# Kernel optimization log

Measured on AMD Instinct MI355X. Metric: run time of the kernel, lower is better.

The kernel has to match this reference:

```python
import jax, jax.numpy as jnp
import numpy as np

D_MODEL = 2048
N_HEADS = 16
D_HEAD = 128
INIT_RANGE = 0.02
EPSILON = -100000.0  # mask fill value from the original module


def setup_inputs() -> dict:
    key = jax.random.key(0)
    ks = jax.random.split(key, 6)
    x = jax.random.normal(ks[0], (2, 2048, D_MODEL), dtype=jnp.float32)
    W_Q = jax.random.normal(ks[1], (N_HEADS, D_MODEL, D_HEAD), dtype=jnp.float32) * INIT_RANGE
    W_K = jax.random.normal(ks[2], (N_HEADS, D_MODEL, D_HEAD), dtype=jnp.float32) * INIT_RANGE
    W_V = jax.random.normal(ks[3], (N_HEADS, D_MODEL, D_HEAD), dtype=jnp.float32) * INIT_RANGE
    W_O = jax.random.normal(ks[4], (N_HEADS, D_HEAD, D_MODEL), dtype=jnp.float32) * INIT_RANGE
    b_Q = jnp.zeros((N_HEADS, D_HEAD), dtype=jnp.float32)
    b_K = jnp.zeros((N_HEADS, D_HEAD), dtype=jnp.float32)
    b_V = jnp.zeros((N_HEADS, D_HEAD), dtype=jnp.float32)
    b_O = jnp.zeros((D_MODEL,), dtype=jnp.float32)
    return {"normalized_resid_pre": x, "W_Q": W_Q, "b_Q": b_Q, "W_K": W_K,
            "b_K": b_K, "W_V": W_V, "b_V": b_V, "W_O": W_O, "b_O": b_O}


def reference(normalized_resid_pre, W_Q, b_Q, W_K, b_K, W_V, b_V, W_O, b_O):
    x = normalized_resid_pre  # [b, s, d_model]
    # per-head projections: [b, s, h, d_head]
    q = jnp.einsum('bsd,hdk->bshk', x, W_Q) + b_Q
    k = jnp.einsum('bsd,hdk->bshk', x, W_K) + b_K
    v = jnp.einsum('bsd,hdk->bshk', x, W_V) + b_V
    # attention scores [b, h, q, k]
    scores = jnp.einsum('bqhk,bshk->bhqs', q, k) / jnp.sqrt(jnp.float32(D_HEAD))
    S = scores.shape[-1]
    causal = jnp.tril(jnp.ones((S, S), dtype=bool))  # True = keep
    scores = jnp.where(causal, scores, jnp.float32(EPSILON))
    pattern = jax.nn.softmax(scores, axis=-1)
    z = jnp.einsum('bhqs,bshk->bqhk', pattern, v)
    attn_out = jnp.einsum('bqhk,hkd->bqd', z, W_O) + b_O
    return attn_out
```

## Files before the change

### kernel.cpp

```cpp
#include <hip/hip_runtime.h>
#include <hip/hip_bf16.h>

typedef unsigned short bfu;
typedef short          bf16x8 __attribute__((ext_vector_type(8)));
typedef float          floatx4 __attribute__((ext_vector_type(4)));
typedef unsigned short bfu4 __attribute__((ext_vector_type(4)));
typedef unsigned int   u32x2 __attribute__((ext_vector_type(2)));

__device__ __forceinline__ bfu f2bf(float f) {
    __hip_bfloat16 h = __float2bfloat16(f);
    return __builtin_bit_cast(unsigned short, h);
}

__device__ __forceinline__ float ex2(float x) {
#if __has_builtin(__builtin_amdgcn_exp2f)
    return __builtin_amdgcn_exp2f(x);
#else
    return exp2f(x);
#endif
}

__device__ __forceinline__ void glds16(const bfu* g, bfu* l) {
    __builtin_amdgcn_global_load_lds(
        (const __attribute__((address_space(1))) unsigned int*)g,
        (__attribute__((address_space(3))) unsigned int*)l, 16, 0, 0);
}

#define BATCH 2
#define SEQ   2048
#define DM    2048
#define NH    16
#define DKH   128
#define SCALE  0.08838834764831845f
#define SCALEQ 0.1275174245f

__global__ __launch_bounds__(256)
void cvt_x(const float* __restrict__ x, bfu* __restrict__ xb, int n) {
    const int i = (blockIdx.x * 256 + threadIdx.x) * 4;
    if (i >= n) return;
    const float4 v = *(const float4*)(x + i);
    bfu4 p; p[0] = f2bf(v.x); p[1] = f2bf(v.y); p[2] = f2bf(v.z); p[3] = f2bf(v.w);
    *(bfu4*)(xb + i) = p;
}

__device__ __forceinline__ void t64(const float* __restrict__ src,
                                    bfu* __restrict__ dst,
                                    int C, int r0, int c0, float s,
                                    float (*tile)[65]) {
    const int t  = threadIdx.x;
    const int lr = t >> 4;
    const int lc = (t & 15) * 4;
    #pragma unroll
    for (int pp = 0; pp < 4; pp++) {
        const float4 v = *(const float4*)(src + (size_t)(r0 + pp*16 + lr) * C + c0 + lc);
        tile[pp*16 + lr][lc + 0] = v.x;
        tile[pp*16 + lr][lc + 1] = v.y;
        tile[pp*16 + lr][lc + 2] = v.z;
        tile[pp*16 + lr][lc + 3] = v.w;
    }
    __syncthreads();
    const int rc = t & 15;
    const int cb = t >> 4;
    #pragma unroll
    for (int pp = 0; pp < 4; pp++) {
        const int c = pp*16 + cb;
        bfu4 pk;
        #pragma unroll
        for (int j = 0; j < 4; j++) pk[j] = f2bf(tile[rc*4 + j][c] * s);
        *(bfu4*)(dst + (size_t)(c0 + c) * DM + r0 + rc*4) = pk;
    }
}

__global__ __launch_bounds__(256)
void tcvt_qkv64(const float* __restrict__ WQ, const float* __restrict__ WK,
                const float* __restrict__ WV,
                bfu* __restrict__ WtQ, bfu* __restrict__ WtK, bfu* __restrict__ WtV) {
    __shared__ float tile[64][65];
    const int z = blockIdx.z;
    const int p = z >> 4, h = z & 15;
    const float* src = ((p == 0) ? WQ : (p == 1) ? WK : WV) + (size_t)h * DM * DKH;
    bfu*         dst = ((p == 0) ? WtQ : (p == 1) ? WtK : WtV) + (size_t)h * DKH * DM;
    const float  s   = (p == 0) ? SCALEQ : 1.0f;
    t64(src, dst, DKH, blockIdx.y * 64, blockIdx.x * 64, s, tile);
}

__global__ __launch_bounds__(256)
void tcvt_wo64(const float* __restrict__ WO, bfu* __restrict__ WtO) {
    __shared__ float tile[64][65];
    t64(WO, WtO, DM, blockIdx.y * 64, blockIdx.x * 64, 1.0f, tile);
}

__device__ __forceinline__ void stg_half(const bfu* gbase, bfu* slot,
                                         int wave, int lane, int csw) {
    #pragma unroll
    for (int l = 0; l < 2; l++) {
        const int j = l * 8 + wave;
        glds16(gbase + (size_t)((j >> 1) * 16 + (lane >> 2)) * DM
                     + (j & 1) * 32 + csw,
               slot + j * 512);
    }
}

__device__ __forceinline__ void ld_b8(bf16x8 (&bv)[4][2], const bfu* slot, int rdo) {
    #pragma unroll
    for (int n = 0; n < 4; n++)
        #pragma unroll
        for (int ks = 0; ks < 2; ks++)
            bv[n][ks] = *(const bf16x8*)&slot[(n * 2 + ks) * 512 + rdo];
}

__device__ __forceinline__ void ld_a8(bf16x8 (&af)[4][2], const bfu* slot, int rdo) {
    #pragma unroll
    for (int m = 0; m < 4; m++)
        #pragma unroll
        for (int ks = 0; ks < 2; ks++)
            af[m][ks] = *(const bf16x8*)&slot[(m * 2 + ks) * 512 + rdo];
}

template<int MH, int NHALF>
__device__ __forceinline__ void mfma16(floatx4 (&acc)[8][4],
                                       const bf16x8 (&af)[4][2],
                                       const bf16x8 (&bv)[4][2]) {
    __builtin_amdgcn_s_setprio(1);
    #pragma unroll
    for (int m = 0; m < 4; m++)
        #pragma unroll
        for (int n = 0; n < 2; n++)
            #pragma unroll
            for (int ks = 0; ks < 2; ks++)
                acc[MH*4 + m][NHALF*2 + n] =
                    __builtin_amdgcn_mfma_f32_16x16x32_bf16(
                        af[m][ks], bv[NHALF*2 + n][ks],
                        acc[MH*4 + m][NHALF*2 + n], 0, 0, 0);
    __builtin_amdgcn_s_setprio(0);
}

#define BARW()                                                      \
    __builtin_amdgcn_s_barrier();                                   \
    asm volatile("s_waitcnt lgkmcnt(0)" ::: "memory");              \
    __builtin_amdgcn_sched_barrier(0)

__global__ __launch_bounds__(512, 2)
void proj_qk8(const bfu* __restrict__ xb,
              const bfu* __restrict__ WtQ, const bfu* __restrict__ WtK,
              const float* __restrict__ bQ, const float* __restrict__ bK,
              bfu* __restrict__ Qall, bfu* __restrict__ Kall) {
    __shared__ __align__(16) bfu As[2][2][8192];
    __shared__ __align__(16) bfu Bs[2][2][8192];

    const int p = blockIdx.y >> 3;
    const bfu*   Wt   = (p == 0) ? WtQ : WtK;
    const float* bias = (p == 0) ? bQ  : bK;
    const float  bscale = (p == 0) ? SCALEQ : 1.0f;

    const int tid  = threadIdx.x;
    const int lane = tid & 63;
    const int wave = tid >> 6;
    const int lrow = lane & 15;
    const int quad = lane >> 4;
    const int wr   = wave >> 2;
    const int wc   = wave & 3;
    const size_t m0 = (size_t)blockIdx.x * 256;
    const int    n0 = (int)(blockIdx.y & 7) * 256;

    const int csw = ((lane & 3) * 8) ^ ((lane & 32) ? 16 : 0);
    const int rdo = lrow * 32 + ((quad * 8) ^ ((lrow & 8) ? 16 : 0));

    const bfu* Ab = xb + m0 * DM;
    const bfu* Bb = Wt + (size_t)n0 * DM;

    floatx4 acc[8][4] = {};
    bf16x8 af[4][2], bv[4][2];

#define STAGE_A(tau, h)                                                     \
    if ((tau) < 32) stg_half(Ab + (size_t)((h) * 128) * DM + (tau) * 64,    \
                             &As[(tau) & 1][h][0], wave, lane, csw)
#define STAGE_B(tau, h)                                                     \
    if ((tau) < 32) stg_half(Bb + (size_t)((h) * 128) * DM + (tau) * 64,    \
                             &Bs[(tau) & 1][h][0], wave, lane, csw)

    STAGE_B(0, 0); STAGE_B(0, 1); STAGE_A(0, 0); STAGE_A(0, 1);
    STAGE_B(1, 0); STAGE_B(1, 1); STAGE_A(1, 0);
    asm volatile("s_waitcnt vmcnt(6)" ::: "memory");
    __builtin_amdgcn_s_barrier();

    #pragma unroll 1
    for (int i = 0; i < 16; i++) {
        const int t0 = 2 * i;
        ld_b8(bv, &Bs[0][wc >> 1][(wc & 1) * 4096], rdo);
        ld_a8(af, &As[0][wr][0], rdo);
        STAGE_A(t0 + 1, 1);
        BARW();
        mfma16<0, 0>(acc, af, bv);
        __builtin_amdgcn_s_barrier();
        STAGE_B(t0 + 2, 0);
        BARW();
        mfma16<0, 1>(acc, af, bv);
        __builtin_amdgcn_s_barrier();
        ld_a8(af, &As[0][wr][4096], rdo);
        STAGE_B(t0 + 2, 1);
        BARW();
        mfma16<1, 0>(acc, af, bv);
        __builtin_amdgcn_s_barrier();
        STAGE_A(t0 + 2, 0);
        BARW();
        mfma16<1, 1>(acc, af, bv);
        if (i == 15) asm volatile("s_waitcnt vmcnt(0)" ::: "memory");
        else         asm volatile("s_waitcnt vmcnt(6)" ::: "memory");
        __builtin_amdgcn_s_barrier();
        ld_b8(bv, &Bs[1][wc >> 1][(wc & 1) * 4096], rdo);
        ld_a8(af, &As[1][wr][0], rdo);
        STAGE_A(t0 + 2, 1);
        BARW();
        mfma16<0, 0>(acc, af, bv);
        __builtin_amdgcn_s_barrier();
        STAGE_B(t0 + 3, 0);
        BARW();
        mfma16<0, 1>(acc, af, bv);
        __builtin_amdgcn_s_barrier();
        ld_a8(af, &As[1][wr][4096], rdo);
        STAGE_B(t0 + 3, 1);
        BARW();
        mfma16<1, 0>(acc, af, bv);
        __builtin_amdgcn_s_barrier();
        STAGE_A(t0 + 3, 0);
        BARW();
        mfma16<1, 1>(acc, af, bv);
        if (i < 15) asm volatile("s_waitcnt vmcnt(6)" ::: "memory");
        __builtin_amdgcn_s_barrier();
    }
#undef STAGE_A
#undef STAGE_B

    bfu* Out = (p == 0) ? Qall : Kall;
    #pragma unroll
    for (int m = 0; m < 8; m++) {
        #pragma unroll
        for (int n = 0; n < 4; n++) {
            const int gn = n0 + wc * 64 + n * 16 + lrow;
            const float bvv = bias[gn] * bscale;
            #pragma unroll
            for (int r = 0; r < 4; r++) {
                const size_t gm = m0 + wr * 128 + m * 16 + quad * 4 + r;
                Out[gm * DM + gn] = f2bf(acc[m][n][r] + bvv);
            }
        }
    }
}

__global__ __launch_bounds__(256)
void proj_v(const bfu* __restrict__ xb, const bfu* __restrict__ WtV,
            const float* __restrict__ bV, bfu* __restrict__ Vt) {
    __shared__ bfu As[128 * 32];
    __shared__ bfu Bs[128 * 32];
    const int tid  = threadIdx.x;
    const int lane = tid & 63;
    const int wave = tid >> 6;
    const int lrow = lane & 15;
    const int quad = lane >> 4;
    const int mw = (wave & 1) * 64;
    const int nw = (wave >> 1) * 64;
    const size_t m0 = (size_t)blockIdx.x * 128;
    const size_t n0 = (size_t)blockIdx.y * 128;
    const int rowb = lane >> 2;
    const int colb = (lane & 3) * 8;

    floatx4 acc[4][4] = {};

    for (int k0 = 0; k0 < DM; k0 += 32) {
        __syncthreads();
        #pragma unroll
        for (int i = 0; i < 2; i++) {
            const int rg = wave * 2 + i;
            glds16(xb  + (m0 + rg*16 + rowb) * DM + k0 + colb, &As[rg * 512]);
            glds16(WtV + (n0 + rg*16 + rowb) * DM + k0 + colb, &Bs[rg * 512]);
        }
        __syncthreads();
        bf16x8 af[4], bfr[4];
        #pragma unroll
        for (int t = 0; t < 4; t++) {
            af[t]  = *(const bf16x8*)&As[(mw + t*16 + lrow) * 32 + quad * 8];
            bfr[t] = *(const bf16x8*)&Bs[(nw + t*16 + lrow) * 32 + quad * 8];
        }
        #pragma unroll
        for (int mt = 0; mt < 4; mt++)
            #pragma unroll
            for (int nt = 0; nt < 4; nt++)
                acc[mt][nt] = __builtin_amdgcn_mfma_f32_16x16x32_bf16(
                                  af[mt], bfr[nt], acc[mt][nt], 0, 0, 0);
    }

    #pragma unroll
    for (int mt = 0; mt < 4; mt++) {
        #pragma unroll
        for (int nt = 0; nt < 4; nt++) {
            const int nl = (int)n0 + nw + nt*16 + lrow;
            const float bvv = bV[nl];
            const size_t gm0 = m0 + mw + mt*16 + quad*4;
            const int b = (int)(gm0 >> 11), s = (int)(gm0 & 2047);
            bfu4 pk;
            #pragma unroll
            for (int r = 0; r < 4; r++) pk[r] = f2bf(acc[mt][nt][r] + bvv);
            *(bfu4*)&Vt[((size_t)(b * NH + (nl >> 7)) * DKH + (nl & 127)) * SEQ + s] = pk;
        }
    }
}

__global__ __launch_bounds__(256)
void flash_attn(const bfu* __restrict__ Q, const bfu* __restrict__ K,
                const bfu* __restrict__ Vt, bfu* __restrict__ Z) {
    __shared__ bfu Ks[4][64][32];
    __shared__ bfu Vs[2][128][32];
    __shared__ bfu Ps[4][16][72];

    const int tid  = threadIdx.x;
    const int lane = tid & 63;
    const int wave = tid >> 6;
    const int lrow = lane & 15;
    const int quad = lane >> 4;
    const int hb = blockIdx.x;
    const int h = hb & 15, b = hb >> 4;
    const int qt = 31 - blockIdx.y;
    const int q0w = qt * 64 + wave * 16;
    const int rowb = lane >> 2;
    const int csw  = ((lane & 3) * 8) ^ ((lane & 32) ? 16 : 0);
    const int rq0  = (quad * 8) ^ ((lrow & 8) ? 16 : 0);

    const bfu* Qrow = Q + (size_t)(b * SEQ + q0w + lrow) * DM + h * DKH;
    bf16x8 qf[4];
    #pragma unroll
    for (int kc = 0; kc < 4; kc++)
        qf[kc] = *(const bf16x8*)(Qrow + kc*32 + quad*8);

    floatx4 z[8] = {};
    float l_loc = 0.f;
    const int qg = q0w + lrow;

    const bfu* Kb = K + (size_t)b * SEQ * DM + h * DKH;
    const bfu* Vb = Vt + (size_t)(b * NH + h) * DKH * SEQ;
    const int ntiles = qt + 1;

    for (int it = 0; it < ntiles; it++) {
        const int s0 = it * 64;
        __syncthreads();
        #pragma unroll
        for (int i = 0; i < 8; i++) {
            const int chunk = wave * 8 + i;
            if (chunk < 16) {
                const int kc = chunk >> 2, kg = chunk & 3;
                glds16(Kb + (size_t)(s0 + kg*16 + rowb) * DM + kc*32 + csw,
                       &Ks[kc][kg*16][0]);
            } else {
                const int c2 = chunk - 16;
                const int sh = c2 >> 3, dg = c2 & 7;
                glds16(Vb + (size_t)(dg*16 + rowb) * SEQ + s0 + sh*32 + csw,
                       &Vs[sh][dg*16][0]);
            }
        }
        __syncthreads();

        floatx4 sc[4];
        __builtin_amdgcn_s_setprio(1);
        #pragma unroll
        for (int st = 0; st < 4; st++) {
            floatx4 a = {};
            #pragma unroll
            for (int kc = 0; kc < 4; kc++) {
                bf16x8 kf = *(const bf16x8*)&Ks[kc][st*16 + lrow][rq0];
                a = __builtin_amdgcn_mfma_f32_16x16x32_bf16(kf, qf[kc], a, 0, 0, 0);
            }
            sc[st] = a;
        }
        __builtin_amdgcn_s_setprio(0);

        if (it + 1 < ntiles) {
            #pragma unroll
            for (int st = 0; st < 4; st++) {
                const float p0 = ex2(sc[st][0]);
                const float p1 = ex2(sc[st][1]);
                const float p2 = ex2(sc[st][2]);
                const float p3 = ex2(sc[st][3]);
                l_loc += (p0 + p1) + (p2 + p3);
                u32x2 pk;
                pk[0] = (unsigned)f2bf(p0) | ((unsigned)f2bf(p1) << 16);
                pk[1] = (unsigned)f2bf(p2) | ((unsigned)f2bf(p3) << 16);
                *(u32x2*)&Ps[wave][lrow][st*16 + quad*4] = pk;
            }
        } else {
            #pragma unroll
            for (int st = 0; st < 4; st++) {
                const int sbase = s0 + st*16 + quad*4;
                const float p0 = (sbase + 0 <= qg) ? ex2(sc[st][0]) : 0.f;
                const float p1 = (sbase + 1 <= qg) ? ex2(sc[st][1]) : 0.f;
                const float p2 = (sbase + 2 <= qg) ? ex2(sc[st][2]) : 0.f;
                const float p3 = (sbase + 3 <= qg) ? ex2(sc[st][3]) : 0.f;
                l_loc += (p0 + p1) + (p2 + p3);
                u32x2 pk;
                pk[0] = (unsigned)f2bf(p0) | ((unsigned)f2bf(p1) << 16);
                pk[1] = (unsigned)f2bf(p2) | ((unsigned)f2bf(p3) << 16);
                *(u32x2*)&Ps[wave][lrow][st*16 + quad*4] = pk;
            }
        }

        bf16x8 pf0 = *(const bf16x8*)&Ps[wave][lrow][quad*8];
        bf16x8 pf1 = *(const bf16x8*)&Ps[wave][lrow][32 + quad*8];
        __builtin_amdgcn_s_setprio(1);
        #pragma unroll
        for (int dt = 0; dt < 8; dt++) {
            bf16x8 v0 = *(const bf16x8*)&Vs[0][dt*16 + lrow][rq0];
            z[dt] = __builtin_amdgcn_mfma_f32_16x16x32_bf16(pf0, v0, z[dt], 0, 0, 0);
            bf16x8 v1 = *(const bf16x8*)&Vs[1][dt*16 + lrow][rq0];
            z[dt] = __builtin_amdgcn_mfma_f32_16x16x32_bf16(pf1, v1, z[dt], 0, 0, 0);
        }
        __builtin_amdgcn_s_setprio(0);
    }

    float L = l_loc;
    L += __shfl_xor(L, 16);
    L += __shfl_xor(L, 32);
    float inv[4];
    #pragma unroll
    for (int r = 0; r < 4; r++)
        inv[r] = 1.0f / __shfl(L, quad*4 + r, 64);
    #pragma unroll
    for (int dt = 0; dt < 8; dt++) {
        #pragma unroll
        for (int r = 0; r < 4; r++) {
            const int qq = q0w + quad*4 + r;
            const int dk = dt*16 + lrow;
            Z[(size_t)(b * SEQ + qq) * DM + h * DKH + dk] = f2bf(z[dt][r] * inv[r]);
        }
    }
}

__global__ __launch_bounds__(256)
void out_gemm(const bfu* __restrict__ Zb, const bfu* __restrict__ WtO,
              const float* __restrict__ bO, float* out) {
    __shared__ bfu As[128 * 32];
    __shared__ bfu Bs[128 * 32];
    const int tid  = threadIdx.x;
    const int lane = tid & 63;
    const int wave = tid >> 6;
    const int lrow = lane & 15;
    const int quad = lane >> 4;
    const int mw = (wave & 1) * 64;
    const int nw = (wave >> 1) * 64;
    const size_t m0 = (size_t)blockIdx.x * 128;
    const size_t n0 = (size_t)blockIdx.y * 128;
    const int rowb = lane >> 2, colb = (lane & 3) * 8;

    floatx4 acc[4][4] = {};

    for (int k0 = 0; k0 < DM; k0 += 32) {
        __syncthreads();
        #pragma unroll
        for (int i = 0; i < 2; i++) {
            const int rg = wave * 2 + i;
            glds16(Zb  + (m0 + rg*16 + rowb) * DM + k0 + colb, &As[rg * 512]);
            glds16(WtO + (n0 + rg*16 + rowb) * DM + k0 + colb, &Bs[rg * 512]);
        }
        __syncthreads();
        bf16x8 af[4], bfr[4];
        #pragma unroll
        for (int t = 0; t < 4; t++) {
            af[t]  = *(const bf16x8*)&As[(mw + t*16 + lrow) * 32 + quad * 8];
            bfr[t] = *(const bf16x8*)&Bs[(nw + t*16 + lrow) * 32 + quad * 8];
        }
        #pragma unroll
        for (int mt = 0; mt < 4; mt++)
            #pragma unroll
            for (int nt = 0; nt < 4; nt++)
                acc[mt][nt] = __builtin_amdgcn_mfma_f32_16x16x32_bf16(
                                  af[mt], bfr[nt], acc[mt][nt], 0, 0, 0);
    }

    #pragma unroll
    for (int mt = 0; mt < 4; mt++) {
        #pragma unroll
        for (int nt = 0; nt < 4; nt++) {
            const size_t gn = n0 + nw + nt*16 + lrow;
            const float bv = bO[gn];
            #pragma unroll
            for (int r = 0; r < 4; r++) {
                const size_t gm = m0 + mw + mt*16 + quad*4 + r;
                out[gm * DM + gn] = acc[mt][nt][r] + bv;
            }
        }
    }
}

extern "C" void kernel_launch(void* const* d_in, const int* in_sizes, int n_in,
                              void* d_out, int out_size, void* d_ws, size_t ws_size,
                              hipStream_t stream) {
    const float* x  = (const float*)d_in[0];
    const float* WQ = (const float*)d_in[1];
    const float* bQ = (const float*)d_in[2];
    const float* WK = (const float*)d_in[3];
    const float* bK = (const float*)d_in[4];
    const float* WV = (const float*)d_in[5];
    const float* bV = (const float*)d_in[6];
    const float* WO = (const float*)d_in[7];
    const float* bO = (const float*)d_in[8];
    float* out = (float*)d_out;
    bfu* ws  = (bfu*)d_ws;
    bfu* dob = (bfu*)d_out;

    bfu* Qall = ws;
    bfu* Kall = Qall + 8388608;
    bfu* Vt   = Kall + 8388608;
    bfu* Zb   = Vt   + 8388608;
    bfu* WtV  = Zb;
    bfu* xb   = dob;
    bfu* WtQ  = dob + 8388608;
    bfu* WtK  = dob + 12582912;

    cvt_x<<<8192, 256, 0, stream>>>(x, xb, BATCH * SEQ * DM);

    tcvt_qkv64<<<dim3(2, 32, 48), 256, 0, stream>>>(WQ, WK, WV, WtQ, WtK, WtV);

    proj_qk8<<<dim3(16, 16), 512, 0, stream>>>(xb, WtQ, WtK, bQ, bK, Qall, Kall);
    proj_v<<<dim3(32, 16), 256, 0, stream>>>(xb, WtV, bV, Vt);

    flash_attn<<<dim3(32, 32), 256, 0, stream>>>(Qall, Kall, Vt, Zb);

    tcvt_wo64<<<dim3(32, 32), 256, 0, stream>>>(WO, Qall);
    out_gemm<<<dim3(32, 16), 256, 0, stream>>>(Zb, Qall, bO, out);
}
```

Measured before the change: 360.6 us.

## Merge input conversion kernels and fuse Q/K/V projections into one launch

Combines the x conversion and the Q/K/V weight transpose-convert into a single `prep` launch, dispatched by block index. It also merges the Q/K projection GEMM and the V projection GEMM into one 512-block `proj_qkv` launch. The V path is retiled to use 512 threads with 128x256 tiles in its own shared buffers. The goal is to cut launch overhead and let the V GEMM run alongside the Q/K GEMM instead of after it. The risk is that the fused kernel's static shared memory grows from 64KB to about 88KB per block, which may stop two blocks from fitting per CU.

```diff
diff --git a/kernel.cpp b/kernel.cpp
--- a/kernel.cpp
+++ b/kernel.cpp
@@ -35,32 +35,39 @@
 #define SCALEQ 0.1275174245f
 
 __global__ __launch_bounds__(256)
-void cvt_x(const float* __restrict__ x, bfu* __restrict__ xb, int n) {
-    const int i = (blockIdx.x * 256 + threadIdx.x) * 4;
-    if (i >= n) return;
-    const float4 v = *(const float4*)(x + i);
-    bfu4 p; p[0] = f2bf(v.x); p[1] = f2bf(v.y); p[2] = f2bf(v.z); p[3] = f2bf(v.w);
-    *(bfu4*)(xb + i) = p;
-}
-
-__device__ __forceinline__ void t64(const float* __restrict__ src,
-                                    bfu* __restrict__ dst,
-                                    int C, int r0, int c0, float s,
-                                    float (*tile)[65]) {
+void prep(const float* __restrict__ x, bfu* __restrict__ xb,
+          const float* __restrict__ WQ, const float* __restrict__ WK,
+          const float* __restrict__ WV,
+          bfu* __restrict__ WtQ, bfu* __restrict__ WtK, bfu* __restrict__ WtV) {
+    __shared__ float tile[64][65];
+    const int bid = blockIdx.x;
+    if (bid < 8192) {
+        const int i = (bid * 256 + threadIdx.x) * 4;
+        const float4 v = *(const float4*)(x + i);
+        bfu4 p; p[0] = f2bf(v.x); p[1] = f2bf(v.y); p[2] = f2bf(v.z); p[3] = f2bf(v.w);
+        *(bfu4*)(xb + i) = p;
+        return;
+    }
+    const int idx = bid - 8192;
+    const int gx = idx & 1, gy = (idx >> 1) & 31, gz = idx >> 6;
+    const int p = gz >> 4, h = gz & 15;
+    const float* src = ((p == 0) ? WQ : (p == 1) ? WK : WV) + (size_t)h * DM * DKH;
+    bfu*         dst = ((p == 0) ? WtQ : (p == 1) ? WtK : WtV) + (size_t)h * DKH * DM;
+    const float  s   = (p == 0) ? SCALEQ : 1.0f;
+    const int r0 = gy * 64, c0 = gx * 64;
     const int t  = threadIdx.x;
     const int lr = t >> 4;
     const int lc = (t & 15) * 4;
     #pragma unroll
     for (int pp = 0; pp < 4; pp++) {
-        const float4 v = *(const float4*)(src + (size_t)(r0 + pp*16 + lr) * C + c0 + lc);
+        const float4 v = *(const float4*)(src + (size_t)(r0 + pp*16 + lr) * DKH + c0 + lc);
         tile[pp*16 + lr][lc + 0] = v.x;
         tile[pp*16 + lr][lc + 1] = v.y;
         tile[pp*16 + lr][lc + 2] = v.z;
         tile[pp*16 + lr][lc + 3] = v.w;
     }
     __syncthreads();
-    const int rc = t & 15;
-    const int cb = t >> 4;
+    const int rc = t & 15, cb = t >> 4;
     #pragma unroll
     for (int pp = 0; pp < 4; pp++) {
         const int c = pp*16 + cb;
@@ -72,22 +79,30 @@
 }
 
 __global__ __launch_bounds__(256)
-void tcvt_qkv64(const float* __restrict__ WQ, const float* __restrict__ WK,
-                const float* __restrict__ WV,
-                bfu* __restrict__ WtQ, bfu* __restrict__ WtK, bfu* __restrict__ WtV) {
-    __shared__ float tile[64][65];
-    const int z = blockIdx.z;
-    const int p = z >> 4, h = z & 15;
-    const float* src = ((p == 0) ? WQ : (p == 1) ? WK : WV) + (size_t)h * DM * DKH;
-    bfu*         dst = ((p == 0) ? WtQ : (p == 1) ? WtK : WtV) + (size_t)h * DKH * DM;
-    const float  s   = (p == 0) ? SCALEQ : 1.0f;
-    t64(src, dst, DKH, blockIdx.y * 64, blockIdx.x * 64, s, tile);
-}
-
-__global__ __launch_bounds__(256)
 void tcvt_wo64(const float* __restrict__ WO, bfu* __restrict__ WtO) {
     __shared__ float tile[64][65];
-    t64(WO, WtO, DM, blockIdx.y * 64, blockIdx.x * 64, 1.0f, tile);
+    const int r0 = blockIdx.y * 64, c0 = blockIdx.x * 64;
+    const int t  = threadIdx.x;
+    const int lr = t >> 4;
+    const int lc = (t & 15) * 4;
+    #pragma unroll
+    for (int pp = 0; pp < 4; pp++) {
+        const float4 v = *(const float4*)(WO + (size_t)(r0 + pp*16 + lr) * DM + c0 + lc);
+        tile[pp*16 + lr][lc + 0] = v.x;
+        tile[pp*16 + lr][lc + 1] = v.y;
+        tile[pp*16 + lr][lc + 2] = v.z;
+        tile[pp*16 + lr][lc + 3] = v.w;
+    }
+    __syncthreads();
+    const int rc = t & 15, cb = t >> 4;
+    #pragma unroll
+    for (int pp = 0; pp < 4; pp++) {
+        const int c = pp*16 + cb;
+        bfu4 pk;
+        #pragma unroll
+        for (int j = 0; j < 4; j++) pk[j] = f2bf(tile[rc*4 + j][c]);
+        *(bfu4*)(WtO + (size_t)(c0 + c) * DM + r0 + rc*4) = pk;
+    }
 }
 
 __device__ __forceinline__ void stg_half(const bfu* gbase, bfu* slot,
@@ -141,36 +156,47 @@
     __builtin_amdgcn_sched_barrier(0)
 
 __global__ __launch_bounds__(512, 2)
-void proj_qk8(const bfu* __restrict__ xb,
+void proj_qkv(const bfu* __restrict__ xb,
               const bfu* __restrict__ WtQ, const bfu* __restrict__ WtK,
+              const bfu* __restrict__ WtV,
               const float* __restrict__ bQ, const float* __restrict__ bK,
-              bfu* __restrict__ Qall, bfu* __restrict__ Kall) {
+              const float* __restrict__ bV,
+              bfu* __restrict__ Qall, bfu* __restrict__ Kall,
+              bfu* __restrict__ Vt) {
     __shared__ __align__(16) bfu As[2][2][8192];
     __shared__ __align__(16) bfu Bs[2][2][8192];
-
-    const int p = blockIdx.y >> 3;
-    const bfu*   Wt   = (p == 0) ? WtQ : WtK;
-    const float* bias = (p == 0) ? bQ  : bK;
-    const float  bscale = (p == 0) ? SCALEQ : 1.0f;
-
+    __shared__ __align__(16) bfu VAs[4096];
+    __shared__ __align__(16) bfu VBs[8192];
+
+    const int bid  = blockIdx.x;
     const int tid  = threadIdx.x;
     const int lane = tid & 63;
     const int wave = tid >> 6;
     const int lrow = lane & 15;
     const int quad = lane >> 4;
-    const int wr   = wave >> 2;
-    const int wc   = wave & 3;
-    const size_t m0 = (size_t)blockIdx.x * 256;
-    const int    n0 = (int)(blockIdx.y & 7) * 256;
-
-    const int csw = ((lane & 3) * 8) ^ ((lane & 32) ? 16 : 0);
-    const int rdo = lrow * 32 + ((quad * 8) ^ ((lrow & 8) ? 16 : 0));
-
-    const bfu* Ab = xb + m0 * DM;
-    const bfu* Bb = Wt + (size_t)n0 * DM;
-
-    floatx4 acc[8][4] = {};
-    bf16x8 af[4][2], bv[4][2];
+    const int rowb = lane >> 2;
+    const int colb = (lane & 3) * 8;
+
+    if (bid < 256) {
+        const int by = bid >> 4;
+        const int p  = by >> 3;
+        const bfu*   Wt   = (p == 0) ? WtQ : WtK;
+        const float* bias = (p == 0) ? bQ  : bK;
+        const float  bscale = (p == 0) ? SCALEQ : 1.0f;
+
+        const int wr   = wave >> 2;
+        const int wc   = wave & 3;
+        const size_t m0 = (size_t)(bid & 15) * 256;
+        const int    n0 = (by & 7) * 256;
+
+        const int csw = ((lane & 3) * 8) ^ ((lane & 32) ? 16 : 0);
+        const int rdo = lrow * 32 + ((quad * 8) ^ ((lrow & 8) ? 16 : 0));
+
+        const bfu* Ab = xb + m0 * DM;
+        const bfu* Bb = Wt + (size_t)n0 * DM;
+
+        floatx4 acc[8][4] = {};
+        bf16x8 af[4][2], bv[4][2];
 
 #define STAGE_A(tau, h)                                                     \
     if ((tau) < 32) stg_half(Ab + (size_t)((h) * 128) * DM + (tau) * 64,    \
@@ -179,108 +205,102 @@
     if ((tau) < 32) stg_half(Bb + (size_t)((h) * 128) * DM + (tau) * 64,    \
                              &Bs[(tau) & 1][h][0], wave, lane, csw)
 
-    STAGE_B(0, 0); STAGE_B(0, 1); STAGE_A(0, 0); STAGE_A(0, 1);
-    STAGE_B(1, 0); STAGE_B(1, 1); STAGE_A(1, 0);
-    asm volatile("s_waitcnt vmcnt(6)" ::: "memory");
-    __builtin_amdgcn_s_barrier();
-
-    #pragma unroll 1
-    for (int i = 0; i < 16; i++) {
-        const int t0 = 2 * i;
-        ld_b8(bv, &Bs[0][wc >> 1][(wc & 1) * 4096], rdo);
-        ld_a8(af, &As[0][wr][0], rdo);
-        STAGE_A(t0 + 1, 1);
-        BARW();
-        mfma16<0, 0>(acc, af, bv);
+        STAGE_B(0, 0); STAGE_B(0, 1); STAGE_A(0, 0); STAGE_A(0, 1);
+        STAGE_B(1, 0); STAGE_B(1, 1); STAGE_A(1, 0);
+        asm volatile("s_waitcnt vmcnt(6)" ::: "memory");
         __builtin_amdgcn_s_barrier();
-        STAGE_B(t0 + 2, 0);
-        BARW();
-        mfma16<0, 1>(acc, af, bv);
-        __builtin_amdgcn_s_barrier();
-        ld_a8(af, &As[0][wr][4096], rdo);
-        STAGE_B(t0 + 2, 1);
-        BARW();
-        mfma16<1, 0>(acc, af, bv);
-        __builtin_amdgcn_s_barrier();
-        STAGE_A(t0 + 2, 0);
-        BARW();
-        mfma16<1, 1>(acc, af, bv);
-        if (i == 15) asm volatile("s_waitcnt vmcnt(0)" ::: "memory");
-        else         asm volatile("s_waitcnt vmcnt(6)" ::: "memory");
-        __builtin_amdgcn_s_barrier();
-        ld_b8(bv, &Bs[1][wc >> 1][(wc & 1) * 4096], rdo);
-        ld_a8(af, &As[1][wr][0], rdo);
-        STAGE_A(t0 + 2, 1);
-        BARW();
-        mfma16<0, 0>(acc, af, bv);
-        __builtin_amdgcn_s_barrier();
-        STAGE_B(t0 + 3, 0);
-        BARW();
-        mfma16<0, 1>(acc, af, bv);
-        __builtin_amdgcn_s_barrier();
-        ld_a8(af, &As[1][wr][4096], rdo);
-        STAGE_B(t0 + 3, 1);
-        BARW();
-        mfma16<1, 0>(acc, af, bv);
-        __builtin_amdgcn_s_barrier();
-        STAGE_A(t0 + 3, 0);
-        BARW();
-        mfma16<1, 1>(acc, af, bv);
-        if (i < 15) asm volatile("s_waitcnt vmcnt(6)" ::: "memory");
-        __builtin_amdgcn_s_barrier();
-    }
+
+        #pragma unroll 1
+        for (int i = 0; i < 16; i++) {
+            const int t0 = 2 * i;
+            ld_b8(bv, &Bs[0][wc >> 1][(wc & 1) * 4096], rdo);
+            ld_a8(af, &As[0][wr][0], rdo);
+            STAGE_A(t0 + 1, 1);
+            BARW();
+            mfma16<0, 0>(acc, af, bv);
+            __builtin_amdgcn_s_barrier();
+            STAGE_B(t0 + 2, 0);
+            BARW();
+            mfma16<0, 1>(acc, af, bv);
+            __builtin_amdgcn_s_barrier();
+            ld_a8(af, &As[0][wr][4096], rdo);
+            STAGE_B(t0 + 2, 1);
+            BARW();
+            mfma16<1, 0>(acc, af, bv);
+            __builtin_amdgcn_s_barrier();
+            STAGE_A(t0 + 2, 0);
+            BARW();
+            mfma16<1, 1>(acc, af, bv);
+            if (i == 15) asm volatile("s_waitcnt vmcnt(0)" ::: "memory");
+            else         asm volatile("s_waitcnt vmcnt(6)" ::: "memory");
+            __builtin_amdgcn_s_barrier();
+            ld_b8(bv, &Bs[1][wc >> 1][(wc & 1) * 4096], rdo);
+            ld_a8(af, &As[1][wr][0], rdo);
+            STAGE_A(t0 + 2, 1);
+            BARW();
+            mfma16<0, 0>(acc, af, bv);
+            __builtin_amdgcn_s_barrier();
+            STAGE_B(t0 + 3, 0);
+            BARW();
+            mfma16<0, 1>(acc, af, bv);
+            __builtin_amdgcn_s_barrier();
+            ld_a8(af, &As[1][wr][4096], rdo);
+            STAGE_B(t0 + 3, 1);
+            BARW();
+            mfma16<1, 0>(acc, af, bv);
+            __builtin_amdgcn_s_barrier();
+            STAGE_A(t0 + 3, 0);
+            BARW();
+            mfma16<1, 1>(acc, af, bv);
+            if (i < 15) asm volatile("s_waitcnt vmcnt(6)" ::: "memory");
+            __builtin_amdgcn_s_barrier();
+        }
 #undef STAGE_A
 #undef STAGE_B
 
-    bfu* Out = (p == 0) ? Qall : Kall;
-    #pragma unroll
-    for (int m = 0; m < 8; m++) {
-        #pragma unroll
-        for (int n = 0; n < 4; n++) {
-            const int gn = n0 + wc * 64 + n * 16 + lrow;
-            const float bvv = bias[gn] * bscale;
-            #pragma unroll
-            for (int r = 0; r < 4; r++) {
-                const size_t gm = m0 + wr * 128 + m * 16 + quad * 4 + r;
-                Out[gm * DM + gn] = f2bf(acc[m][n][r] + bvv);
-            }
-        }
-    }
-}
-
-__global__ __launch_bounds__(256)
-void proj_v(const bfu* __restrict__ xb, const bfu* __restrict__ WtV,
-            const float* __restrict__ bV, bfu* __restrict__ Vt) {
-    __shared__ bfu As[128 * 32];
-    __shared__ bfu Bs[128 * 32];
-    const int tid  = threadIdx.x;
-    const int lane = tid & 63;
-    const int wave = tid >> 6;
-    const int lrow = lane & 15;
-    const int quad = lane >> 4;
+        bfu* Out = (p == 0) ? Qall : Kall;
+        #pragma unroll
+        for (int m = 0; m < 8; m++) {
+            #pragma unroll
+            for (int n = 0; n < 4; n++) {
+                const int gn = n0 + wc * 64 + n * 16 + lrow;
+                const float bvv = bias[gn] * bscale;
+                #pragma unroll
+                for (int r = 0; r < 4; r++) {
+                    const size_t gm = m0 + wr * 128 + m * 16 + quad * 4 + r;
+                    Out[gm * DM + gn] = f2bf(acc[m][n][r] + bvv);
+                }
+            }
+        }
+        return;
+    }
+
+    const int vb = bid - 256;
+    const size_t m0 = (size_t)(vb & 31) * 128;
+    const size_t n0 = (size_t)(vb >> 5) * 256;
     const int mw = (wave & 1) * 64;
     const int nw = (wave >> 1) * 64;
-    const size_t m0 = (size_t)blockIdx.x * 128;
-    const size_t n0 = (size_t)blockIdx.y * 128;
-    const int rowb = lane >> 2;
-    const int colb = (lane & 3) * 8;
 
     floatx4 acc[4][4] = {};
 
     for (int k0 = 0; k0 < DM; k0 += 32) {
         __syncthreads();
         #pragma unroll
-        for (int i = 0; i < 2; i++) {
-            const int rg = wave * 2 + i;
-            glds16(xb  + (m0 + rg*16 + rowb) * DM + k0 + colb, &As[rg * 512]);
-            glds16(WtV + (n0 + rg*16 + rowb) * DM + k0 + colb, &Bs[rg * 512]);
+        for (int j = 0; j < 3; j++) {
+            const int c = wave * 3 + j;
+            if (c < 8) {
+                glds16(xb  + (m0 + c*16 + rowb) * DM + k0 + colb, &VAs[c * 512]);
+            } else {
+                const int c2 = c - 8;
+                glds16(WtV + (n0 + c2*16 + rowb) * DM + k0 + colb, &VBs[c2 * 512]);
+            }
         }
         __syncthreads();
         bf16x8 af[4], bfr[4];
         #pragma unroll
         for (int t = 0; t < 4; t++) {
-            af[t]  = *(const bf16x8*)&As[(mw + t*16 + lrow) * 32 + quad * 8];
-            bfr[t] = *(const bf16x8*)&Bs[(nw + t*16 + lrow) * 32 + quad * 8];
+            af[t]  = *(const bf16x8*)&VAs[(mw + t*16 + lrow) * 32 + quad * 8];
+            bfr[t] = *(const bf16x8*)&VBs[(nw + t*16 + lrow) * 32 + quad * 8];
         }
         #pragma unroll
         for (int mt = 0; mt < 4; mt++)
@@ -514,12 +534,10 @@
     bfu* WtQ  = dob + 8388608;
     bfu* WtK  = dob + 12582912;
 
-    cvt_x<<<8192, 256, 0, stream>>>(x, xb, BATCH * SEQ * DM);
-
-    tcvt_qkv64<<<dim3(2, 32, 48), 256, 0, stream>>>(WQ, WK, WV, WtQ, WtK, WtV);
-
-    proj_qk8<<<dim3(16, 16), 512, 0, stream>>>(xb, WtQ, WtK, bQ, bK, Qall, Kall);
-    proj_v<<<dim3(32, 16), 256, 0, stream>>>(xb, WtV, bV, Vt);
+    prep<<<11264, 256, 0, stream>>>(x, xb, WQ, WK, WV, WtQ, WtK, WtV);
+
+    proj_qkv<<<512, 512, 0, stream>>>(xb, WtQ, WtK, WtV, bQ, bK, bV,
+                                      Qall, Kall, Vt);
 
     flash_attn<<<dim3(32, 32), 256, 0, stream>>>(Qall, Kall, Vt, Zb);
 
```

Result: slower. 369.2 us (+2.4%).
